# Performance work log

Hardware: AMD Instinct MI355X
Metric: run time of the kernel (lower is better)

## Reference

```python
import jax, jax.numpy as jnp
import numpy as np

P = 8  # patch size


def setup_inputs() -> dict:
    key = jax.random.key(0)
    k0, k1, k2, k3 = jax.random.split(key, 4)
    B, Cin, H, W = 4, 96, 256, 256
    hid = 192
    C2 = hid * 2
    x = jax.random.normal(k0, (B, Cin, H, W), jnp.float32)
    # project_in: 1x1 conv, no bias -> weight [C2, Cin]
    w_in = jax.random.normal(k1, (C2, Cin), jnp.float32) * 0.05
    # dwconv: 3x3 depthwise, groups=C2 -> weight [C2, 1, 3, 3]
    w_dw = jax.random.normal(k2, (C2, 1, 3, 3), jnp.float32) * 0.05
    # spectral gate parameter, initialized to ones as in the torch module
    fft_w = jnp.ones((C2, 1, 1, P, P // 2 + 1), jnp.float32)
    # project_out: 1x1 conv hid -> Cin
    w_out = jax.random.normal(k3, (Cin, hid), jnp.float32) * 0.05
    return {"x": x, "w_in": w_in, "w_dw": w_dw, "fft_w": fft_w, "w_out": w_out}


def reference(x, w_in, w_dw, fft_w, w_out):
    B, Cin, H, W = x.shape
    C2 = w_in.shape[0]
    # project_in (1x1 conv == channel GEMM)
    x = jnp.einsum('oc,bchw->bohw', w_in, x)
    # patchwise rearrange: b c (h p1) (w p2) -> b c h w p1 p2
    h, w = H // P, W // P
    xp = x.reshape(B, C2, h, P, w, P).transpose(0, 1, 2, 4, 3, 5)
    # spectral gate on each 8x8 patch
    xf = jnp.fft.rfft2(xp) * fft_w  # fft_w [C2,1,1,8,5] broadcasts over b,h,w
    xp = jnp.fft.irfft2(xf, s=(P, P))
    # rearrange back: b c h w p1 p2 -> b c (h p1) (w p2)
    x = xp.transpose(0, 1, 2, 4, 3, 5).reshape(B, C2, H, W)
    # 3x3 depthwise conv, padding=1
    x = jax.lax.conv_general_dilated(
        x, w_dw, window_strides=(1, 1), padding='SAME',
        feature_group_count=C2,
        dimension_numbers=('NCHW', 'OIHW', 'NCHW'))
    # GELU gating (exact erf gelu, matching torch F.gelu default)
    x1, x2 = jnp.split(x, 2, axis=1)
    x = jax.nn.gelu(x1, approximate=False) * x2
    # project_out (1x1 conv)
    return jnp.einsum('oc,bchw->bohw', w_out, x)
```

## Files before the change

kernel.cpp:

```cpp
#include <hip/hip_runtime.h>
#include <hip/hip_bf16.h>
#include <math.h>

typedef short bf16x8 __attribute__((ext_vector_type(8)));
typedef float f32x4  __attribute__((ext_vector_type(4)));

constexpr int B_=4, CIN=96, H_=256, W_=256, HID=192, C2=384;
constexpr int NPX = H_*W_;
#define PB 8
constexpr int HP = H_/PB, WP = W_/PB;

__device__ __forceinline__ ushort f2bf(float f) {
    __hip_bfloat16 h = __float2bfloat16(f);
    ushort u; __builtin_memcpy(&u, &h, 2); return u;
}
__device__ __forceinline__ float bf2f(ushort u) {
    __hip_bfloat16 h; __builtin_memcpy(&h, &u, 2); return __bfloat162float(h);
}
__device__ __forceinline__ float extc(uint u, int sub) {
    uint w = sub ? (u & 0xffff0000u) : (u << 16);
    float f; __builtin_memcpy(&f, &w, 4); return f;
}

__device__ __forceinline__ float gelu_f(float x) {
    float u  = x * 0.70710678118654752f;
    float au = fabsf(u);
    float t  = __builtin_amdgcn_rcpf(fmaf(0.3275911f, au, 1.0f));
    float poly = t * fmaf(t, fmaf(t, fmaf(t, fmaf(t, 1.061405429f,
                     -1.453152027f), 1.421413741f), -0.284496736f),
                     0.254829592f);
    float e  = __builtin_amdgcn_exp2f(au * au * -1.4426950408889634f);
    float g  = fmaf(-poly, e, 1.0f);
    float one_plus = 1.0f + copysignf(g, u);
    return 0.5f * x * one_plus;
}

__global__ void prep_gate(const float* __restrict__ fftw,
                          float* __restrict__ g, int* __restrict__ flags) {
    int c = blockIdx.x;
    int t = threadIdx.x;
    int n1 = t >> 3, n2 = t & 7;
    const float* Wc = fftw + c * 40;
    const double ct[8] = {1.0, 0.70710678118654752, 0.0, -0.70710678118654752,
                          -1.0, -0.70710678118654752, 0.0, 0.70710678118654752};
    double acc = 0.0;
    for (int k1 = 0; k1 < 8; ++k1)
        for (int k2 = 0; k2 < 8; ++k2) {
            double geff;
            if (k2 == 0 || k2 == 4)
                geff = 0.5 * ((double)Wc[k1*5+k2] + (double)Wc[((8-k1)&7)*5+k2]);
            else if (k2 < 4) geff = (double)Wc[k1*5+k2];
            else             geff = (double)Wc[((8-k1)&7)*5 + (8-k2)];
            acc += geff * ct[(k1*n1 + k2*n2) & 7];
        }
    acc *= (1.0/64.0);
    g[c*64 + t] = (float)acc;
    double expect = (t == 0) ? 1.0 : 0.0;
    unsigned long long m = __ballot(fabs(acc - expect) <= 1e-6);
    if (t == 0) flags[c] = (m == 0xFFFFFFFFFFFFFFFFull) ? 1 : 0;
}

__global__ void reduce_flags(const int* __restrict__ flags,
                             int* __restrict__ allflag) {
    int t = threadIdx.x;
    int ok = 1;
    for (int j = t; j < C2; j += 64) ok &= flags[j];
    unsigned long long m = __ballot(ok != 0);
    if (t == 0) allflag[0] = (m == 0xFFFFFFFFFFFFFFFFull) ? 1 : 0;
}

__global__ void prep_fragw(const float* __restrict__ w_in,
                           const float* __restrict__ w_out,
                           ushort* __restrict__ wfin,
                           ushort* __restrict__ wfout) {
    int idx = blockIdx.x * 256 + threadIdx.x;
    if (idx < 72 * 64) {
        int f = idx >> 6, l = idx & 63;
        int wv = f / 9, rem = f % 9;
        int kc = rem / 3, mf = rem % 3;
        int row = wv*48 + mf*16 + (l & 15);
        int kb  = kc*32 + (l >> 4)*8;
        ushort* dst = wfin + (size_t)f*1024 + l*16;
#pragma unroll
        for (int j = 0; j < 8; ++j) {
            float v = w_in[(size_t)row*CIN + kb + j];
            ushort h = f2bf(v);
            dst[j]   = h;
            dst[8+j] = f2bf(v - bf2f(h));
        }
    }
    int jdx = idx - 72*64;
    if (jdx >= 0 && jdx < 36 * 64) {
        int f = jdx >> 6, l = jdx & 63;
        int ocg = f / 18, rem = f % 18;
        int kc = rem / 3, mf = rem % 3;
        int row = ocg*48 + mf*16 + (l & 15);
        int kb  = kc*32 + (l >> 4)*8;
        ushort* dst = wfout + (size_t)f*1024 + l*16;
#pragma unroll
        for (int j = 0; j < 8; ++j) {
            float v = w_out[(size_t)row*HID + kb + j];
            ushort h = f2bf(v);
            dst[j]   = h;
            dst[8+j] = f2bf(v - bf2f(h));
        }
    }
}

__global__ __launch_bounds__(512)
void gemm1_mfma(const float* __restrict__ x,
                const ushort* __restrict__ wfin,
                uint* __restrict__ z4, int b0) {
    __shared__ uint lds[96*68];
    int t = threadIdx.x;
    int l = t & 63, wv = t >> 6;
    int lm = l & 15, g4 = l >> 4;
    int px0 = blockIdx.x * 64;
    int r0 = px0 >> 8, c0 = px0 & 255;
    int bg = blockIdx.y;
    const float* xb = x + (size_t)(b0 + bg) * CIN * NPX;
    uint* zb = z4 + (size_t)bg * HID * NPX;

    for (int i = t; i < 768; i += 512) {
        int cp = i >> 4;
        int q  = i & 15;
        const float* pa = xb + (size_t)(2*cp) * NPX + px0 + 4*q;
        float4 a = *(const float4*)pa;
        float4 b = *(const float4*)(pa + NPX);
        lds[(4*q+0)*53 + cp] = (uint)f2bf(a.x) | ((uint)f2bf(b.x) << 16);
        lds[(4*q+1)*53 + cp] = (uint)f2bf(a.y) | ((uint)f2bf(b.y) << 16);
        lds[(4*q+2)*53 + cp] = (uint)f2bf(a.z) | ((uint)f2bf(b.z) << 16);
        lds[(4*q+3)*53 + cp] = (uint)f2bf(a.w) | ((uint)f2bf(b.w) << 16);
    }
    __syncthreads();

    f32x4 acc[3][4];
#pragma unroll
    for (int mf = 0; mf < 3; ++mf)
#pragma unroll
        for (int nf = 0; nf < 4; ++nf) acc[mf][nf] = (f32x4){0.f,0.f,0.f,0.f};

#pragma unroll
    for (int kc = 0; kc < 3; ++kc) {
        int cp0 = kc*16 + g4*4;
        bf16x8 bfr[4];
#pragma unroll
        for (int nf = 0; nf < 4; ++nf)
            bfr[nf] = *(const bf16x8*)&lds[(nf*16 + lm)*53 + cp0];
#pragma unroll
        for (int mf = 0; mf < 3; ++mf) {
            int f = wv*9 + kc*3 + mf;
            const ushort* wp = wfin + (size_t)f*1024 + l*16;
            bf16x8 ah = *(const bf16x8*)wp;
            bf16x8 al = *(const bf16x8*)(wp + 8);
#pragma unroll
            for (int nf = 0; nf < 4; ++nf) {
                acc[mf][nf] = __builtin_amdgcn_mfma_f32_16x16x32_bf16(ah, bfr[nf], acc[mf][nf], 0,0,0);
                acc[mf][nf] = __builtin_amdgcn_mfma_f32_16x16x32_bf16(al, bfr[nf], acc[mf][nf], 0,0,0);
            }
        }
    }

#pragma unroll
    for (int ph = 0; ph < 2; ++ph) {
        __syncthreads();
        if ((wv >> 2) == ph) {
            int wl = wv & 3;
#pragma unroll
            for (int mf = 0; mf < 3; ++mf)
#pragma unroll
                for (int nf = 0; nf < 4; ++nf) {
                    int col = nf*16 + lm;
                    int lr  = wl*24 + mf*8 + g4*2;
                    lds[lr*68 + col]     = (uint)f2bf(acc[mf][nf][0]) |
                                           ((uint)f2bf(acc[mf][nf][1]) << 16);
                    lds[(lr+1)*68 + col] = (uint)f2bf(acc[mf][nf][2]) |
                                           ((uint)f2bf(acc[mf][nf][3]) << 16);
                }
        }
        __syncthreads();
#pragma unroll
        for (int i = 0; i < 3; ++i) {
            int idx = t + i*512;
            int lr = idx >> 4, q = idx & 15;
            uint4 v = *(const uint4*)&lds[lr*68 + 4*q];
            *(uint4*)(zb + ((size_t)r0*192 + ph*96 + lr) * 256 + c0 + 4*q) = v;
        }
    }
}

__global__ __launch_bounds__(256)
void gate_fix(uint* __restrict__ z4, const float* __restrict__ g,
              const int* __restrict__ flags, const int* __restrict__ allflag) {
    if (allflag[0]) return;
    int pid = blockIdx.x;
    int bg = blockIdx.y;
    int ph = pid >> 5, pw = pid & 31;
    int t = threadIdx.x, l = t & 63, wv = t >> 6;
    int p1 = l >> 3, p2 = l & 7;
    uint* zb = z4 + (size_t)bg * HID * NPX;
    for (int cp = wv; cp < HID; cp += 4) {
        int f0 = flags[2*cp], f1 = flags[2*cp+1];
        if (f0 & f1) continue;
        const float* gc0 = g + (2*cp)*64;
        const float* gc1 = gc0 + 64;
        size_t zi = ((size_t)(ph*8 + p1) * 192 + cp) * 256 + pw*8 + p2;
        uint u = zb[zi];
        float v0 = extc(u, 0), v1 = extc(u, 1);
        float s0 = 0.f, s1 = 0.f;
        for (int q = 0; q < 64; ++q) {
            int idx = ((p1 - (q >> 3)) & 7)*8 + ((p2 - (q & 7)) & 7);
            s0 += __shfl(v0, q, 64) * gc0[idx];
            s1 += __shfl(v1, q, 64) * gc1[idx];
        }
        float r0 = f0 ? v0 : s0;
        float r1 = f1 ? v1 : s1;
        zb[zi] = (uint)f2bf(r0) | ((uint)f2bf(r1) << 16);
    }
}

constexpr int DROWS = 8;
__global__ __launch_bounds__(256)
void dw_gelu6(const uint* __restrict__ z4, const float* __restrict__ w_dw,
              uint* __restrict__ tg4) {
    int t = threadIdx.x;
    int wv = t >> 6, lane = t & 63;
    int strip = blockIdx.x * 4 + wv;
    int s = blockIdx.y;
    int jg = s >> 2, pp = s & 3;
    int bg = blockIdx.z;
    int row0 = strip * DROWS;
    int cb = lane * 4;
    const uint* zb = z4 + (size_t)bg * HID * NPX;
    uint* tb = tg4 + (size_t)bg * HID/2 * NPX;

    int c  = jg*8 + pp*2;
    int p1 = c >> 1;
    int p2 = p1 + 96;
    float wA[18], wB[18];
#pragma unroll
    for (int k = 0; k < 18; ++k) {
        wA[k] = w_dw[(size_t)c*9 + k];
        wB[k] = w_dw[(size_t)(c+HID)*9 + k];
    }

    float accA[2][2][4], accB[2][2][4];
#pragma unroll
    for (int sx = 0; sx < 2; ++sx)
#pragma unroll
        for (int u = 0; u < 2; ++u)
#pragma unroll
            for (int j = 0; j < 4; ++j) { accA[sx][u][j]=0.f; accB[sx][u][j]=0.f; }

    auto ld = [&](int r, uint4& A, uint4& B) {
        int y = row0 - 1 + r;
        A = (uint4){0,0,0,0}; B = (uint4){0,0,0,0};
        if (y >= 0 && y < H_) {
            A = *(const uint4*)(zb + ((size_t)y*192 + p1)*256 + cb);
            B = *(const uint4*)(zb + ((size_t)y*192 + p2)*256 + cb);
        }
    };

    uint4 a_cur, b_cur;
    ld(0, a_cur, b_cur);
#pragma unroll
    for (int r = 0; r < DROWS + 2; ++r) {
        uint4 a_nxt, b_nxt;
        if (r < DROWS + 1) ld(r + 1, a_nxt, b_nxt);

        uint aL = (uint)__shfl_up((int)a_cur.w, 1, 64);  if (lane == 0)  aL = 0u;
        uint aR = (uint)__shfl_down((int)a_cur.x, 1, 64); if (lane == 63) aR = 0u;
        uint bL = (uint)__shfl_up((int)b_cur.w, 1, 64);  if (lane == 0)  bL = 0u;
        uint bR = (uint)__shfl_down((int)b_cur.x, 1, 64); if (lane == 63) bR = 0u;

        float dA[2][4], dB[2][4];
#pragma unroll
        for (int sub = 0; sub < 2; ++sub) {
            {
                float xv[6] = {extc(aL,sub), extc(a_cur.x,sub), extc(a_cur.y,sub),
                               extc(a_cur.z,sub), extc(a_cur.w,sub), extc(aR,sub)};
                const float* w = &wA[sub*9];
#pragma unroll
                for (int j = 0; j < 4; ++j) {
                    float h2 = fmaf(xv[j],w[6], fmaf(xv[j+1],w[7], xv[j+2]*w[8]));
                    float h1 = fmaf(xv[j],w[3], fmaf(xv[j+1],w[4], xv[j+2]*w[5]));
                    float h0 = fmaf(xv[j],w[0], fmaf(xv[j+1],w[1], xv[j+2]*w[2]));
                    dA[sub][j]    = accA[0][sub][j] + h2;
                    accA[0][sub][j] = accB[0][sub][j] + h1;
                    accB[0][sub][j] = h0;
                }
            }
            {
                float xv[6] = {extc(bL,sub), extc(b_cur.x,sub), extc(b_cur.y,sub),
                               extc(b_cur.z,sub), extc(b_cur.w,sub), extc(bR,sub)};
                const float* w = &wB[sub*9];
#pragma unroll
                for (int j = 0; j < 4; ++j) {
                    float h2 = fmaf(xv[j],w[6], fmaf(xv[j+1],w[7], xv[j+2]*w[8]));
                    float h1 = fmaf(xv[j],w[3], fmaf(xv[j+1],w[4], xv[j+2]*w[5]));
                    float h0 = fmaf(xv[j],w[0], fmaf(xv[j+1],w[1], xv[j+2]*w[2]));
                    dB[sub][j]    = accA[1][sub][j] + h2;
                    accA[1][sub][j] = accB[1][sub][j] + h1;
                    accB[1][sub][j] = h0;
                }
            }
        }

        if (r >= 2) {
            int o = row0 + r - 2;
            uint4 val;
            val.x = (uint)f2bf(gelu_f(dA[0][0]) * dB[0][0]) |
                    (((uint)f2bf(gelu_f(dA[1][0]) * dB[1][0])) << 16);
            val.y = (uint)f2bf(gelu_f(dA[0][1]) * dB[0][1]) |
                    (((uint)f2bf(gelu_f(dA[1][1]) * dB[1][1])) << 16);
            val.z = (uint)f2bf(gelu_f(dA[0][2]) * dB[0][2]) |
                    (((uint)f2bf(gelu_f(dA[1][2]) * dB[1][2])) << 16);
            val.w = (uint)f2bf(gelu_f(dA[0][3]) * dB[0][3]) |
                    (((uint)f2bf(gelu_f(dA[1][3]) * dB[1][3])) << 16);
            *(uint4*)(tb + ((size_t)o*96 + s)*256 + cb) = val;
        }
        a_cur = a_nxt; b_cur = b_nxt;
    }
}

__global__ __launch_bounds__(512)
void gemm2_mfma(const uint* __restrict__ tg4,
                const ushort* __restrict__ wfout,
                float* __restrict__ out, int b0) {
    __shared__ float os[32][260];
    int t = threadIdx.x;
    int l = t & 63, wv = t >> 6;
    int ocg = wv & 1, pxg = wv >> 1;
    int lm = l & 15, g4 = l >> 4;
    int h = blockIdx.x;
    int bg = blockIdx.z;
    const uint* tb = tg4 + (size_t)bg * HID/2 * NPX;

    f32x4 acc[3][4];
#pragma unroll
    for (int mf = 0; mf < 3; ++mf)
#pragma unroll
        for (int nf = 0; nf < 4; ++nf) acc[mf][nf] = (f32x4){0.f,0.f,0.f,0.f};

#pragma unroll
    for (int kc = 0; kc < 6; ++kc) {
        int s0 = kc*16 + g4*4;
        bf16x8 bfr[4];
#pragma unroll
        for (int nf = 0; nf < 4; ++nf) {
            int col = pxg*64 + nf*16 + lm;
            uint4 u;
            u.x = tb[((size_t)h*96 + s0+0)*256 + col];
            u.y = tb[((size_t)h*96 + s0+1)*256 + col];
            u.z = tb[((size_t)h*96 + s0+2)*256 + col];
            u.w = tb[((size_t)h*96 + s0+3)*256 + col];
            bf16x8 v; __builtin_memcpy(&v, &u, 16);
            bfr[nf] = v;
        }
#pragma unroll
        for (int mf = 0; mf < 3; ++mf) {
            int f = ocg*18 + kc*3 + mf;
            const ushort* wp = wfout + (size_t)f*1024 + l*16;
            bf16x8 ah = *(const bf16x8*)wp;
            bf16x8 al = *(const bf16x8*)(wp + 8);
#pragma unroll
            for (int nf = 0; nf < 4; ++nf) {
                acc[mf][nf] = __builtin_amdgcn_mfma_f32_16x16x32_bf16(ah, bfr[nf], acc[mf][nf], 0,0,0);
                acc[mf][nf] = __builtin_amdgcn_mfma_f32_16x16x32_bf16(al, bfr[nf], acc[mf][nf], 0,0,0);
            }
        }
    }
    float* ob = out + (size_t)(b0 + bg) * CIN * NPX;
#pragma unroll
    for (int mf = 0; mf < 3; ++mf) {
        if (mf) __syncthreads();
#pragma unroll
        for (int nf = 0; nf < 4; ++nf) {
            int col = pxg*64 + nf*16 + lm;
#pragma unroll
            for (int r = 0; r < 4; ++r)
                os[ocg*16 + g4*4 + r][col] = acc[mf][nf][r];
        }
        __syncthreads();
#pragma unroll
        for (int ri = 0; ri < 4; ++ri) {
            int idx = t + ri*512;
            int ro = idx >> 6, l4 = idx & 63;
            int oc = mf*16 + (ro & 15) + (ro >> 4)*48;
            f32x4 v = *(const f32x4*)&os[ro][l4*4];
            __builtin_nontemporal_store(v,
                (f32x4*)(ob + (size_t)oc*NPX + (size_t)h*W_ + l4*4));
        }
    }
}

extern "C" void kernel_launch(void* const* d_in, const int* in_sizes, int n_in,
                              void* d_out, int out_size, void* d_ws, size_t ws_size,
                              hipStream_t stream) {
    const float* x     = (const float*)d_in[0];
    const float* w_in  = (const float*)d_in[1];
    const float* w_dw  = (const float*)d_in[2];
    const float* fftw  = (const float*)d_in[3];
    const float* w_out = (const float*)d_in[4];
    float* out = (float*)d_out;

    char* ws = (char*)d_ws;
    ushort* wfin   = (ushort*)(ws + 0);
    ushort* wfout  = (ushort*)(ws + 147456);
    float*  g      = (float*) (ws + 221184);
    int*    flags  = (int*)   (ws + 319488);
    int*    allflag= (int*)   (ws + 321024);

    const size_t zoff   = 327680;
    const size_t zbytes = (size_t)HID * NPX * 4;
    const size_t tbytes = (size_t)(HID/2) * NPX * 4;
    size_t avail = (ws_size > zoff) ? ws_size - zoff : 0;
    int nbg = (int)(avail / (zbytes + tbytes));
    if (nbg < 1) nbg = 1;
    if (nbg > 2) nbg = 2;
    uint* z4  = (uint*)(ws + zoff);
    uint* tg4 = (uint*)(ws + zoff + (size_t)nbg * zbytes);

    prep_gate<<<dim3(C2), dim3(64), 0, stream>>>(fftw, g, flags);
    reduce_flags<<<dim3(1), dim3(64), 0, stream>>>(flags, allflag);
    prep_fragw<<<dim3(27), dim3(256), 0, stream>>>(w_in, w_out, wfin, wfout);

    for (int b0 = 0; b0 < B_; b0 += nbg) {
        int nb = (B_ - b0 < nbg) ? (B_ - b0) : nbg;
        gemm1_mfma<<<dim3(NPX/64, nb), dim3(512), 0, stream>>>(x, wfin, z4, b0);
        gate_fix<<<dim3(HP*WP, nb), dim3(256), 0, stream>>>(z4, g, flags, allflag);
        dw_gelu6<<<dim3(H_/DROWS/4, 96, nb), dim3(256), 0, stream>>>(z4, w_dw, tg4);
        gemm2_mfma<<<dim3(H_, 1, nb), dim3(512), 0, stream>>>(tg4, wfout, out, b0);
    }
}
```

Measured before the change: 191.8 us.

## Fuse depthwise conv + GELU gating into project_out GEMM via LDS

Merges the depthwise 3x3 conv/GELU-gate kernel with the second MFMA GEMM so that each block computes one image row of gated activations for all 96 channel pairs into shared memory, then runs the output projection directly from LDS. This removes the global write and re-read of the intermediate tg buffer and one kernel launch per batch group. In exchange, each row block re-reads the three neighbouring z rows (3x vertical reloading instead of the sliding-window reuse), uses about 133KB of dynamic LDS per block (limiting occupancy), and loads depthwise weights from global inside the loop.

```diff
diff --git a/kernel.cpp b/kernel.cpp
--- a/kernel.cpp
+++ b/kernel.cpp
@@ -219,123 +219,73 @@
     }
 }
 
-constexpr int DROWS = 8;
-__global__ __launch_bounds__(256)
-void dw_gelu6(const uint* __restrict__ z4, const float* __restrict__ w_dw,
-              uint* __restrict__ tg4) {
+__global__ __launch_bounds__(512)
+void dwg2(const uint* __restrict__ z4, const float* __restrict__ w_dw,
+          const ushort* __restrict__ wfout, float* __restrict__ out, int b0) {
+    extern __shared__ uint smem[];
+    uint  (*tgs)[260] = (uint(*)[260])smem;
+    float (*os)[260]  = (float(*)[260])(smem + 96*260);
     int t = threadIdx.x;
-    int wv = t >> 6, lane = t & 63;
-    int strip = blockIdx.x * 4 + wv;
-    int s = blockIdx.y;
-    int jg = s >> 2, pp = s & 3;
+    int l = t & 63, wv = t >> 6;
+    int h = blockIdx.x;
     int bg = blockIdx.z;
-    int row0 = strip * DROWS;
-    int cb = lane * 4;
     const uint* zb = z4 + (size_t)bg * HID * NPX;
-    uint* tb = tg4 + (size_t)bg * HID/2 * NPX;
-
-    int c  = jg*8 + pp*2;
-    int p1 = c >> 1;
-    int p2 = p1 + 96;
-    float wA[18], wB[18];
-#pragma unroll
-    for (int k = 0; k < 18; ++k) {
-        wA[k] = w_dw[(size_t)c*9 + k];
-        wB[k] = w_dw[(size_t)(c+HID)*9 + k];
-    }
-
-    float accA[2][2][4], accB[2][2][4];
-#pragma unroll
-    for (int sx = 0; sx < 2; ++sx)
-#pragma unroll
-        for (int u = 0; u < 2; ++u)
-#pragma unroll
-            for (int j = 0; j < 4; ++j) { accA[sx][u][j]=0.f; accB[sx][u][j]=0.f; }
-
-    auto ld = [&](int r, uint4& A, uint4& B) {
-        int y = row0 - 1 + r;
-        A = (uint4){0,0,0,0}; B = (uint4){0,0,0,0};
-        if (y >= 0 && y < H_) {
-            A = *(const uint4*)(zb + ((size_t)y*192 + p1)*256 + cb);
-            B = *(const uint4*)(zb + ((size_t)y*192 + p2)*256 + cb);
-        }
-    };
-
-    uint4 a_cur, b_cur;
-    ld(0, a_cur, b_cur);
-#pragma unroll
-    for (int r = 0; r < DROWS + 2; ++r) {
-        uint4 a_nxt, b_nxt;
-        if (r < DROWS + 1) ld(r + 1, a_nxt, b_nxt);
-
-        uint aL = (uint)__shfl_up((int)a_cur.w, 1, 64);  if (lane == 0)  aL = 0u;
-        uint aR = (uint)__shfl_down((int)a_cur.x, 1, 64); if (lane == 63) aR = 0u;
-        uint bL = (uint)__shfl_up((int)b_cur.w, 1, 64);  if (lane == 0)  bL = 0u;
-        uint bR = (uint)__shfl_down((int)b_cur.x, 1, 64); if (lane == 63) bR = 0u;
-
-        float dA[2][4], dB[2][4];
-#pragma unroll
-        for (int sub = 0; sub < 2; ++sub) {
-            {
-                float xv[6] = {extc(aL,sub), extc(a_cur.x,sub), extc(a_cur.y,sub),
-                               extc(a_cur.z,sub), extc(a_cur.w,sub), extc(aR,sub)};
-                const float* w = &wA[sub*9];
+
+    int cb = l * 4;
+#pragma unroll
+    for (int i = 0; i < 12; ++i) {
+        int q = wv*12 + i;
+        int c2 = 2*q;
+        const float* wA_ = w_dw + (size_t)c2*9;
+        const float* wB_ = w_dw + (size_t)(c2+HID)*9;
+        float d1[2][4] = {{0.f,0.f,0.f,0.f},{0.f,0.f,0.f,0.f}};
+        float d2[2][4] = {{0.f,0.f,0.f,0.f},{0.f,0.f,0.f,0.f}};
+#pragma unroll
+        for (int r = 0; r < 3; ++r) {
+            int y = h - 1 + r;
+            uint4 A = (uint4){0,0,0,0}, Bv = (uint4){0,0,0,0};
+            if (y >= 0 && y < H_) {
+                A  = *(const uint4*)(zb + ((size_t)y*192 + q     )*256 + cb);
+                Bv = *(const uint4*)(zb + ((size_t)y*192 + q + 96)*256 + cb);
+            }
+            uint aL = (uint)__shfl_up((int)A.w, 1, 64);    if (l == 0)  aL = 0u;
+            uint aR = (uint)__shfl_down((int)A.x, 1, 64);  if (l == 63) aR = 0u;
+            uint bL = (uint)__shfl_up((int)Bv.w, 1, 64);   if (l == 0)  bL = 0u;
+            uint bR = (uint)__shfl_down((int)Bv.x, 1, 64); if (l == 63) bR = 0u;
+#pragma unroll
+            for (int sub = 0; sub < 2; ++sub) {
+                float xa[6] = {extc(aL,sub), extc(A.x,sub), extc(A.y,sub),
+                               extc(A.z,sub), extc(A.w,sub), extc(aR,sub)};
+                float xc[6] = {extc(bL,sub), extc(Bv.x,sub), extc(Bv.y,sub),
+                               extc(Bv.z,sub), extc(Bv.w,sub), extc(bR,sub)};
+                const float* w1 = wA_ + sub*9 + r*3;
+                const float* w2 = wB_ + sub*9 + r*3;
+                float u0 = w1[0], u1 = w1[1], u2 = w1[2];
+                float v0 = w2[0], v1 = w2[1], v2 = w2[2];
 #pragma unroll
                 for (int j = 0; j < 4; ++j) {
-                    float h2 = fmaf(xv[j],w[6], fmaf(xv[j+1],w[7], xv[j+2]*w[8]));
-                    float h1 = fmaf(xv[j],w[3], fmaf(xv[j+1],w[4], xv[j+2]*w[5]));
-                    float h0 = fmaf(xv[j],w[0], fmaf(xv[j+1],w[1], xv[j+2]*w[2]));
-                    dA[sub][j]    = accA[0][sub][j] + h2;
-                    accA[0][sub][j] = accB[0][sub][j] + h1;
-                    accB[0][sub][j] = h0;
+                    d1[sub][j] = fmaf(xa[j],u0, fmaf(xa[j+1],u1,
+                                  fmaf(xa[j+2],u2, d1[sub][j])));
+                    d2[sub][j] = fmaf(xc[j],v0, fmaf(xc[j+1],v1,
+                                  fmaf(xc[j+2],v2, d2[sub][j])));
                 }
             }
-            {
-                float xv[6] = {extc(bL,sub), extc(b_cur.x,sub), extc(b_cur.y,sub),
-                               extc(b_cur.z,sub), extc(b_cur.w,sub), extc(bR,sub)};
-                const float* w = &wB[sub*9];
-#pragma unroll
-                for (int j = 0; j < 4; ++j) {
-                    float h2 = fmaf(xv[j],w[6], fmaf(xv[j+1],w[7], xv[j+2]*w[8]));
-                    float h1 = fmaf(xv[j],w[3], fmaf(xv[j+1],w[4], xv[j+2]*w[5]));
-                    float h0 = fmaf(xv[j],w[0], fmaf(xv[j+1],w[1], xv[j+2]*w[2]));
-                    dB[sub][j]    = accA[1][sub][j] + h2;
-                    accA[1][sub][j] = accB[1][sub][j] + h1;
-                    accB[1][sub][j] = h0;
-                }
-            }
-        }
-
-        if (r >= 2) {
-            int o = row0 + r - 2;
-            uint4 val;
-            val.x = (uint)f2bf(gelu_f(dA[0][0]) * dB[0][0]) |
-                    (((uint)f2bf(gelu_f(dA[1][0]) * dB[1][0])) << 16);
-            val.y = (uint)f2bf(gelu_f(dA[0][1]) * dB[0][1]) |
-                    (((uint)f2bf(gelu_f(dA[1][1]) * dB[1][1])) << 16);
-            val.z = (uint)f2bf(gelu_f(dA[0][2]) * dB[0][2]) |
-                    (((uint)f2bf(gelu_f(dA[1][2]) * dB[1][2])) << 16);
-            val.w = (uint)f2bf(gelu_f(dA[0][3]) * dB[0][3]) |
-                    (((uint)f2bf(gelu_f(dA[1][3]) * dB[1][3])) << 16);
-            *(uint4*)(tb + ((size_t)o*96 + s)*256 + cb) = val;
-        }
-        a_cur = a_nxt; b_cur = b_nxt;
-    }
-}
-
-__global__ __launch_bounds__(512)
-void gemm2_mfma(const uint* __restrict__ tg4,
-                const ushort* __restrict__ wfout,
-                float* __restrict__ out, int b0) {
-    __shared__ float os[32][260];
-    int t = threadIdx.x;
-    int l = t & 63, wv = t >> 6;
+        }
+        uint4 val;
+        val.x = (uint)f2bf(gelu_f(d1[0][0])*d2[0][0]) |
+                (((uint)f2bf(gelu_f(d1[1][0])*d2[1][0])) << 16);
+        val.y = (uint)f2bf(gelu_f(d1[0][1])*d2[0][1]) |
+                (((uint)f2bf(gelu_f(d1[1][1])*d2[1][1])) << 16);
+        val.z = (uint)f2bf(gelu_f(d1[0][2])*d2[0][2]) |
+                (((uint)f2bf(gelu_f(d1[1][2])*d2[1][2])) << 16);
+        val.w = (uint)f2bf(gelu_f(d1[0][3])*d2[0][3]) |
+                (((uint)f2bf(gelu_f(d1[1][3])*d2[1][3])) << 16);
+        *(uint4*)&tgs[q][cb] = val;
+    }
+    __syncthreads();
+
+    int lm = l & 15, g4 = l >> 4;
     int ocg = wv & 1, pxg = wv >> 1;
-    int lm = l & 15, g4 = l >> 4;
-    int h = blockIdx.x;
-    int bg = blockIdx.z;
-    const uint* tb = tg4 + (size_t)bg * HID/2 * NPX;
-
     f32x4 acc[3][4];
 #pragma unroll
     for (int mf = 0; mf < 3; ++mf)
@@ -350,10 +300,10 @@
         for (int nf = 0; nf < 4; ++nf) {
             int col = pxg*64 + nf*16 + lm;
             uint4 u;
-            u.x = tb[((size_t)h*96 + s0+0)*256 + col];
-            u.y = tb[((size_t)h*96 + s0+1)*256 + col];
-            u.z = tb[((size_t)h*96 + s0+2)*256 + col];
-            u.w = tb[((size_t)h*96 + s0+3)*256 + col];
+            u.x = tgs[s0+0][col];
+            u.y = tgs[s0+1][col];
+            u.z = tgs[s0+2][col];
+            u.w = tgs[s0+3][col];
             bf16x8 v; __builtin_memcpy(&v, &u, 16);
             bfr[nf] = v;
         }
@@ -373,7 +323,7 @@
     float* ob = out + (size_t)(b0 + bg) * CIN * NPX;
 #pragma unroll
     for (int mf = 0; mf < 3; ++mf) {
-        if (mf) __syncthreads();
+        __syncthreads();
 #pragma unroll
         for (int nf = 0; nf < 4; ++nf) {
             int col = pxg*64 + nf*16 + lm;
@@ -413,23 +363,22 @@
 
     const size_t zoff   = 327680;
     const size_t zbytes = (size_t)HID * NPX * 4;
-    const size_t tbytes = (size_t)(HID/2) * NPX * 4;
     size_t avail = (ws_size > zoff) ? ws_size - zoff : 0;
-    int nbg = (int)(avail / (zbytes + tbytes));
+    int nbg = (int)(avail / zbytes);
     if (nbg < 1) nbg = 1;
     if (nbg > 2) nbg = 2;
-    uint* z4  = (uint*)(ws + zoff);
-    uint* tg4 = (uint*)(ws + zoff + (size_t)nbg * zbytes);
+    uint* z4 = (uint*)(ws + zoff);
 
     prep_gate<<<dim3(C2), dim3(64), 0, stream>>>(fftw, g, flags);
     reduce_flags<<<dim3(1), dim3(64), 0, stream>>>(flags, allflag);
     prep_fragw<<<dim3(27), dim3(256), 0, stream>>>(w_in, w_out, wfin, wfout);
+
+    const size_t dwg2_lds = (size_t)(96 + 32) * 260 * 4;
 
     for (int b0 = 0; b0 < B_; b0 += nbg) {
         int nb = (B_ - b0 < nbg) ? (B_ - b0) : nbg;
         gemm1_mfma<<<dim3(NPX/64, nb), dim3(512), 0, stream>>>(x, wfin, z4, b0);
         gate_fix<<<dim3(HP*WP, nb), dim3(256), 0, stream>>>(z4, g, flags, allflag);
-        dw_gelu6<<<dim3(H_/DROWS/4, 96, nb), dim3(256), 0, stream>>>(z4, w_dw, tg4);
-        gemm2_mfma<<<dim3(H_, 1, nb), dim3(512), 0, stream>>>(tg4, wfout, out, b0);
-    }
-}
+        dwg2<<<dim3(H_, 1, nb), dim3(512), dwg2_lds, stream>>>(z4, w_dw, wfout, out, b0);
+    }
+}
```

Result: slower. 231.5 us (+20.7%).
